# Optimization experiments

Hardware: AMD Instinct MI355X
Metric: run time of the kernel (lower is better)

## Reference

```python
import jax, jax.numpy as jnp
import numpy as np

N = 100000   # nodes
E = 1600000  # edges (avg degree 16)
DIM = 3      # coordinate dims
R = 3        # pseudo-coordinate dim
C = 32       # channels / Gaussian kernels
F = 64       # non-coordinate node features


def setup_inputs() -> dict:
    key = jax.random.key(0)
    k1, k2, k3, k4, k5 = jax.random.split(key, 5)
    features = jax.random.normal(k1, (N, DIM + F), dtype=jnp.float32)
    edge_index = jax.random.randint(k2, (E, 2), 0, N, dtype=jnp.int32)  # (row=i, col=j) per edge
    w_dense = jax.random.normal(k3, (DIM, R), dtype=jnp.float32) / jnp.sqrt(jnp.float32(DIM))  # lecun-ish
    b_dense = jnp.zeros((R,), dtype=jnp.float32)
    mu = jax.random.normal(k4, (C, N, R), dtype=jnp.float32) * 0.1
    # sigma initialized positive (abs of lecun normal in the original); keep bounded away from 0
    sig = jax.random.uniform(k5, (C, N, R), dtype=jnp.float32, minval=0.1, maxval=1.0)
    return {"features": features, "edge_index": edge_index,
            "w_dense": w_dense, "b_dense": b_dense, "mu": mu, "sig": sig}


def reference(features, edge_index, w_dense, b_dense, mu, sig):
    coords = features[:, :DIM]          # [N, 3]
    h = features[:, DIM:]               # [N, F]
    src = edge_index[:, 0]              # row index i per edge
    dst = edge_index[:, 1]              # col index j per edge
    # per-edge pseudo-coordinates: tanh(Dense_r(x_j - x_i))
    u = jnp.tanh((coords[dst] - coords[src]) @ w_dense + b_dense)      # [E, R]
    # Gaussian-mixture edge weight per (channel, edge), mu/sigma gathered at row node i
    diff = u[None, :, :] - mu[:, src, :]                               # [C, E, R]
    w = jnp.exp(-0.5 * jnp.sum(diff * diff / sig[:, src, :], axis=-1)) # [C, E]
    # (A o W) @ H summed over feature axis == sum_j w[c,i,j] * sum_f H[j,f]
    msg = w * jnp.sum(h, axis=-1)[dst][None, :]                        # [C, E]
    agg = jax.ops.segment_sum(msg.T, src, num_segments=N)              # [N, C]
    return jnp.concatenate([coords, agg], axis=-1)                     # [N, DIM + C]
```

## Files before the change

### kernel.cpp

```cpp
#include <hip/hip_runtime.h>

#define DIMV 3
#define RV 3
#define CV 32
#define ROWF 67
#define ROWO 35
#define CAP 48
#define PADSTR 49
#define SCAN_T 1024
#define NGRP 8
#define BSH 5
#define BNODES 32
#define SEGCAP 192
#define CCH 8
#define MSPAD 97

__device__ __forceinline__ float fast_tanh(float x) {
    float ex = __expf(2.0f * x);
    return (ex - 1.0f) * __builtin_amdgcn_rcpf(ex + 1.0f);
}

__device__ __forceinline__ int xcc_id() {
    int x;
    asm("s_getreg_b32 %0, hwreg(HW_REG_XCC_ID)" : "=s"(x));
    return x & (NGRP - 1);
}

__global__ void prep_kernel(const float* __restrict__ features,
                            float4* __restrict__ nd,
                            int* __restrict__ counts,
                            int* __restrict__ bcur, int nbc,
                            float* __restrict__ out, int N) {
    int gid = blockIdx.x * blockDim.x + threadIdx.x;
    if (gid < N) counts[gid] = 0;
    if (gid < nbc) bcur[gid] = 0;
    int node = gid >> 6;
    int lane = threadIdx.x & 63;
    if (node >= N) return;
    const float* row = features + (size_t)node * ROWF;
    float f0 = row[lane];
    float f1 = (lane < ROWF - 64) ? row[64 + lane] : 0.0f;
    float v = (lane >= DIMV ? f0 : 0.0f) + f1;
    for (int off = 32; off > 0; off >>= 1) v += __shfl_xor(v, off, 64);
    float c0 = __shfl(f0, 0, 64);
    float c1 = __shfl(f0, 1, 64);
    float c2 = __shfl(f0, 2, 64);
    if (lane == 0) nd[node] = make_float4(c0, c1, c2, v);
    if (lane < DIMV) out[(size_t)node * ROWO + lane] = f0;
}

__global__ void bin_kernel(const int2* __restrict__ ei2,
                           int* __restrict__ bcur,
                           unsigned int* __restrict__ bins, int E, int NB) {
    int grp = xcc_id();
    int stride = gridDim.x * blockDim.x;
    for (int e = blockIdx.x * blockDim.x + threadIdx.x; e < E; e += stride) {
        unsigned long long v =
            __builtin_nontemporal_load((const unsigned long long*)ei2 + e);
        int s = (int)(v & 0xffffffffull);
        int d = (int)(v >> 32);
        int b = s >> BSH;
        int g = grp;
        int slot = atomicAdd(bcur + g * NB + b, 1);
#pragma unroll 1
        for (int tries = 0; slot >= SEGCAP && tries < NGRP; ++tries) {
            g = (g + 1) & (NGRP - 1);
            slot = atomicAdd(bcur + g * NB + b, 1);
        }
        if (slot < SEGCAP)
            bins[(size_t)(g * NB + b) * SEGCAP + slot] =
                ((unsigned)(s & (BNODES - 1)) << 17) | (unsigned)d;
    }
}

__global__ __launch_bounds__(256, 5)
void fused_bucket_kernel(const int* __restrict__ bcur,
                         const unsigned int* __restrict__ bins,
                         const float4* __restrict__ nd,
                         const float* __restrict__ wd,
                         const float* __restrict__ bd,
                         const float* __restrict__ mu,
                         const float* __restrict__ sig,
                         float* __restrict__ out, int N, int NB) {
    __shared__ float4 ue[BNODES * PADSTR];
    __shared__ float4 snd[BNODES];
    __shared__ int lcnt[BNODES];
    __shared__ int soff[NGRP + 1];
    __shared__ float msm[CCH * MSPAD];
    __shared__ float mss[CCH * MSPAD];
    int b = blockIdx.x;
    int base = b << BSH;
    int nn = N - base; if (nn > BNODES) nn = BNODES;
    int t = threadIdx.x;
    if (t < BNODES) {
        lcnt[t] = 0;
        snd[t] = (t < nn) ? nd[base + t] : make_float4(0.f, 0.f, 0.f, 0.f);
    }
    if (t < NGRP) {
        int c = bcur[t * NB + b];
        soff[t + 1] = (c > SEGCAP) ? SEGCAP : c;
    }
    if (t == 0) soff[0] = 0;
    __syncthreads();
    if (t == 0) {
#pragma unroll
        for (int g = 0; g < NGRP; ++g) soff[g + 1] += soff[g];
    }
    __syncthreads();
    float w0 = wd[0], w1 = wd[1], w2 = wd[2];
    float w3 = wd[3], w4 = wd[4], w5 = wd[5];
    float w6 = wd[6], w7 = wd[7], w8 = wd[8];
    float b0 = bd[0], b1 = bd[1], b2 = bd[2];
    int total = soff[NGRP];
    for (int r = t; r < total; r += 256) {
        int g = 0;
#pragma unroll
        for (int gg = 1; gg < NGRP; ++gg) if (r >= soff[gg]) g = gg;
        int i = r - soff[g];
        unsigned p = bins[(size_t)(g * NB + b) * SEGCAP + i];
        int sl = p >> 17;
        int d  = p & 0x1FFFF;
        float4 pd = nd[d];
        int k = atomicAdd(&lcnt[sl], 1);
        if (k >= CAP) k = CAP - 1;
        float4 ps = snd[sl];
        float dx = pd.x - ps.x, dy = pd.y - ps.y, dz = pd.z - ps.z;
        float u0 = fast_tanh(dx * w0 + dy * w3 + dz * w6 + b0);
        float u1 = fast_tanh(dx * w1 + dy * w4 + dz * w7 + b1);
        float u2 = fast_tanh(dx * w2 + dy * w5 + dz * w8 + b2);
        ue[sl * PADSTR + k] = make_float4(u0, u1, u2, pd.w);
    }
    __syncthreads();
    int c8 = t & (CCH - 1);
    int n  = t >> 3;
    size_t slab = (size_t)N * RV;
    int cnt = 0;
    if (n < nn) { cnt = lcnt[n]; if (cnt > CAP) cnt = CAP; }
    for (int cc = 0; cc < CV / CCH; ++cc) {
        for (int f = t; f < CCH * RV * BNODES; f += 256) {
            int ci = f / (RV * BNODES);
            int j  = f - ci * (RV * BNODES);
            float vm = 0.0f, vs = 1.0f;
            if (j < nn * RV) {
                size_t gidx = (size_t)(cc * CCH + ci) * slab + (size_t)base * RV + j;
                vm = mu[gidx];
                vs = sig[gidx];
            }
            msm[ci * MSPAD + j] = vm;
            mss[ci * MSPAD + j] = vs;
        }
        __syncthreads();
        if (n < nn) {
            const float* mrow = &msm[c8 * MSPAD + n * RV];
            const float* srow = &mss[c8 * MSPAD + n * RV];
            float m0 = mrow[0], m1 = mrow[1], m2 = mrow[2];
            float i0 = __builtin_amdgcn_rcpf(srow[0]);
            float i1 = __builtin_amdgcn_rcpf(srow[1]);
            float i2 = __builtin_amdgcn_rcpf(srow[2]);
            float acc = 0.0f;
            for (int k = 0; k < cnt; ++k) {
                float4 q = ue[n * PADSTR + k];
                float d0 = q.x - m0, d1 = q.y - m1, d2 = q.z - m2;
                float t2 = d0 * d0 * i0 + d1 * d1 * i1 + d2 * d2 * i2;
                acc += __expf(-0.5f * t2) * q.w;
            }
            out[(size_t)(base + n) * ROWO + DIMV + cc * CCH + c8] = acc;
        }
        __syncthreads();
    }
}


__global__ void hist_kernel(const int2* __restrict__ ei2, int* __restrict__ counts, int E) {
    int e = blockIdx.x * blockDim.x + threadIdx.x;
    if (e >= E) return;
    atomicAdd(counts + ei2[e].x, 1);
}

__global__ void scan_a_kernel(const int* __restrict__ counts, int* __restrict__ offsets,
                              int* __restrict__ partials, int N) {
    __shared__ int sm[SCAN_T];
    int t = threadIdx.x;
    int i = blockIdx.x * SCAN_T + t;
    int c = (i < N) ? counts[i] : 0;
    sm[t] = c;
    __syncthreads();
    for (int off = 1; off < SCAN_T; off <<= 1) {
        int v = (t >= off) ? sm[t - off] : 0;
        __syncthreads();
        sm[t] += v;
        __syncthreads();
    }
    if (i < N) offsets[i] = sm[t] - c;
    if (t == SCAN_T - 1) partials[blockIdx.x] = sm[t];
}

__global__ void scan_b_kernel(int* __restrict__ partials, int B) {
    __shared__ int sm[SCAN_T];
    int t = threadIdx.x;
    int c = (t < B) ? partials[t] : 0;
    sm[t] = c;
    __syncthreads();
    for (int off = 1; off < SCAN_T; off <<= 1) {
        int v = (t >= off) ? sm[t - off] : 0;
        __syncthreads();
        sm[t] += v;
        __syncthreads();
    }
    if (t < B) partials[t] = sm[t] - c;
}

__global__ void scan_c_kernel(int* __restrict__ offsets, const int* __restrict__ partials,
                              int* __restrict__ cursor, int N, int E) {
    int i = blockIdx.x * blockDim.x + threadIdx.x;
    if (i == 0) offsets[N] = E;
    if (i >= N) return;
    int off = offsets[i] + partials[i / SCAN_T];
    offsets[i] = off;
    cursor[i] = off;
}

__global__ void scatter_u_kernel(const int2* __restrict__ ei2, int* __restrict__ cursor,
                                 const float4* __restrict__ nd,
                                 const float* __restrict__ wd, const float* __restrict__ bd,
                                 float4* __restrict__ ue, int E) {
    int e = blockIdx.x * blockDim.x + threadIdx.x;
    if (e >= E) return;
    int2 sd = ei2[e];
    int pos = atomicAdd(cursor + sd.x, 1);
    float4 ps = nd[sd.x];
    float4 pd = nd[sd.y];
    float dx = pd.x - ps.x, dy = pd.y - ps.y, dz = pd.z - ps.z;
    float u0 = fast_tanh(dx * wd[0] + dy * wd[3] + dz * wd[6] + bd[0]);
    float u1 = fast_tanh(dx * wd[1] + dy * wd[4] + dz * wd[7] + bd[1]);
    float u2 = fast_tanh(dx * wd[2] + dy * wd[5] + dz * wd[8] + bd[2]);
    ue[pos] = make_float4(u0, u1, u2, pd.w);
}

__global__ void node_acc2_kernel(const int* __restrict__ offsets,
                                 const float4* __restrict__ ue,
                                 const float* __restrict__ mu,
                                 const float* __restrict__ sig,
                                 float* __restrict__ out, int N) {
    int node = (blockIdx.x * blockDim.x + threadIdx.x) >> 6;
    if (node >= N) return;
    int lane = threadIdx.x & 63;
    int c = lane & 31;
    int half = lane >> 5;
    size_t slab = (size_t)N * RV;
    const float* mp = mu + (size_t)c * slab + (size_t)node * RV;
    const float* sp = sig + (size_t)c * slab + (size_t)node * RV;
    float m0 = mp[0], m1 = mp[1], m2 = mp[2];
    float i0 = __builtin_amdgcn_rcpf(sp[0]);
    float i1 = __builtin_amdgcn_rcpf(sp[1]);
    float i2 = __builtin_amdgcn_rcpf(sp[2]);
    int off0 = offsets[node], off1 = offsets[node + 1];
    float acc = 0.0f;
    for (int i = off0 + half; i < off1; i += 2) {
        float4 q = ue[i];
        float d0 = q.x - m0, d1 = q.y - m1, d2 = q.z - m2;
        float t = d0 * d0 * i0 + d1 * d1 * i1 + d2 * d2 * i2;
        acc += __expf(-0.5f * t) * q.w;
    }
    acc += __shfl_xor(acc, 32, 64);
    if (half == 0) out[(size_t)node * ROWO + DIMV + c] = acc;
}


__global__ void fb_pre_kernel(const float* __restrict__ features,
                              float4* __restrict__ nd, float* __restrict__ out, int N) {
    int gid = blockIdx.x * blockDim.x + threadIdx.x;
    int node = gid >> 6;
    int lane = threadIdx.x & 63;
    if (node >= N) return;
    const float* row = features + (size_t)node * ROWF;
    float f0 = row[lane];
    float f1 = (lane < ROWF - 64) ? row[64 + lane] : 0.0f;
    float v = (lane >= DIMV ? f0 : 0.0f) + f1;
    for (int off = 32; off > 0; off >>= 1) v += __shfl_xor(v, off, 64);
    float c0 = __shfl(f0, 0, 64);
    float c1 = __shfl(f0, 1, 64);
    float c2 = __shfl(f0, 2, 64);
    if (lane == 0) nd[node] = make_float4(c0, c1, c2, v);
    float* orow = out + (size_t)node * ROWO;
    if (lane < DIMV) orow[lane] = f0;
    else if (lane < ROWO) orow[lane] = 0.0f;
}

__global__ void fb_edge_kernel(const int* __restrict__ ei, const float4* __restrict__ nd,
                               const float* __restrict__ wd, const float* __restrict__ bd,
                               const float* __restrict__ mu, const float* __restrict__ sig,
                               float* __restrict__ out, int N, int E) {
    int e = blockIdx.x * blockDim.x + threadIdx.x;
    if (e >= E) return;
    int s = ei[2 * e];
    int d = ei[2 * e + 1];
    float4 ps = nd[s];
    float4 pd = nd[d];
    float dx = pd.x - ps.x, dy = pd.y - ps.y, dz = pd.z - ps.z;
    float u0 = fast_tanh(dx * wd[0] + dy * wd[3] + dz * wd[6] + bd[0]);
    float u1 = fast_tanh(dx * wd[1] + dy * wd[4] + dz * wd[7] + bd[1]);
    float u2 = fast_tanh(dx * wd[2] + dy * wd[5] + dz * wd[8] + bd[2]);
    float hs = pd.w;
    float* oagg = out + (size_t)s * ROWO + DIMV;
    size_t nodeoff = (size_t)s * RV;
    size_t slab = (size_t)N * RV;
#pragma unroll 4
    for (int c = 0; c < CV; ++c) {
        const float* mp = mu + (size_t)c * slab + nodeoff;
        const float* sp = sig + (size_t)c * slab + nodeoff;
        float d0 = u0 - mp[0], d1 = u1 - mp[1], d2 = u2 - mp[2];
        float t = d0 * d0 * __builtin_amdgcn_rcpf(sp[0])
                + d1 * d1 * __builtin_amdgcn_rcpf(sp[1])
                + d2 * d2 * __builtin_amdgcn_rcpf(sp[2]);
        atomicAdd(oagg + c, __expf(-0.5f * t) * hs);
    }
}

extern "C" void kernel_launch(void* const* d_in, const int* in_sizes, int n_in,
                              void* d_out, int out_size, void* d_ws, size_t ws_size,
                              hipStream_t stream) {
    const float* features = (const float*)d_in[0];
    const int*   ei       = (const int*)d_in[1];
    const int2*  ei2      = (const int2*)d_in[1];
    const float* wd       = (const float*)d_in[2];
    const float* bd       = (const float*)d_in[3];
    const float* mu       = (const float*)d_in[4];
    const float* sig      = (const float*)d_in[5];
    float* out = (float*)d_out;

    int N = in_sizes[0] / ROWF;
    int E = in_sizes[1] / 2;
    int B = (N + SCAN_T - 1) / SCAN_T;
    int NB = (N + BNODES - 1) / BNODES;

    size_t cur = 0;
    auto take = [&](size_t bytes) { size_t p = cur; cur += (bytes + 255) & ~(size_t)255; return p; };
    size_t o_nd      = take((size_t)N * sizeof(float4));
    size_t o_counts  = take((size_t)N * sizeof(int));
    size_t o_offsets = take((size_t)(N + 1) * sizeof(int));
    size_t o_cursor  = take((size_t)N * sizeof(int));
    size_t o_part    = take((size_t)SCAN_T * sizeof(int));
    size_t o_bcur    = take((size_t)NGRP * NB * sizeof(int));
    size_t o_bins    = take((size_t)NGRP * NB * SEGCAP * sizeof(unsigned int));
    size_t o_tail    = cur;
    size_t need_fused = o_tail;
    size_t need_full  = o_tail + (((size_t)E * sizeof(float4) + 255) & ~(size_t)255);

    char* ws = (char*)d_ws;
    float4* nd   = (float4*)(ws + o_nd);
    int* counts  = (int*)(ws + o_counts);
    int* offsets = (int*)(ws + o_offsets);
    int* cursor  = (int*)(ws + o_cursor);
    int* part    = (int*)(ws + o_part);
    int* bcur    = (int*)(ws + o_bcur);
    unsigned int* bins = (unsigned int*)(ws + o_bins);

    if (ws_size >= need_fused && N < (1 << 17)) {
        prep_kernel<<<(N + 3) / 4, 256, 0, stream>>>(features, nd, counts, bcur, NGRP * NB, out, N);
        bin_kernel<<<2048, 256, 0, stream>>>(ei2, bcur, bins, E, NB);
        fused_bucket_kernel<<<NB, 256, 0, stream>>>(bcur, bins, nd, wd, bd, mu, sig, out, N, NB);
    } else if (ws_size >= need_full && B <= SCAN_T) {
        float4* ue = (float4*)(ws + o_tail);
        prep_kernel<<<(N + 3) / 4, 256, 0, stream>>>(features, nd, counts, bcur, 0, out, N);
        hist_kernel<<<(E + 255) / 256, 256, 0, stream>>>(ei2, counts, E);
        scan_a_kernel<<<B, SCAN_T, 0, stream>>>(counts, offsets, part, N);
        scan_b_kernel<<<1, SCAN_T, 0, stream>>>(part, B);
        scan_c_kernel<<<(N + 255) / 256, 256, 0, stream>>>(offsets, part, cursor, N, E);
        scatter_u_kernel<<<(E + 255) / 256, 256, 0, stream>>>(ei2, cursor, nd, wd, bd, ue, E);
        node_acc2_kernel<<<(N + 3) / 4, 256, 0, stream>>>(offsets, ue, mu, sig, out, N);
    } else {
        fb_pre_kernel<<<(N + 3) / 4, 256, 0, stream>>>(features, nd, out, N);
        fb_edge_kernel<<<(E + 255) / 256, 256, 0, stream>>>(ei, nd, wd, bd, mu, sig, out, N, E);
    }
}
```

Measured before the change: 278.1 us.

## Compute four channels per thread with direct mu/sig loads, dropping LDS staging loop

The Gaussian-mixture phase no longer stages mu/sig through shared memory in four channel chunks with barriers. Each thread now loads its node's mu/sig for four channels straight from global memory and reuses every edge record read from shared memory across those four channels. Edge slots are XOR-swizzled by node group to cut LDS bank conflicts, and the occupancy hint rises from 5 to 6 waves. The cost is more registers per thread, and global mu/sig loads that are strided and less coalesced than the old cooperative staging.

```diff
diff --git a/kernel.cpp b/kernel.cpp
--- a/kernel.cpp
+++ b/kernel.cpp
@@ -12,8 +12,6 @@
 #define BSH 5
 #define BNODES 32
 #define SEGCAP 192
-#define CCH 8
-#define MSPAD 97
 
 __device__ __forceinline__ float fast_tanh(float x) {
     float ex = __expf(2.0f * x);
@@ -73,7 +71,7 @@
     }
 }
 
-__global__ __launch_bounds__(256, 5)
+__global__ __launch_bounds__(256, 6)
 void fused_bucket_kernel(const int* __restrict__ bcur,
                          const unsigned int* __restrict__ bins,
                          const float4* __restrict__ nd,
@@ -86,8 +84,6 @@
     __shared__ float4 snd[BNODES];
     __shared__ int lcnt[BNODES];
     __shared__ int soff[NGRP + 1];
-    __shared__ float msm[CCH * MSPAD];
-    __shared__ float mss[CCH * MSPAD];
     int b = blockIdx.x;
     int base = b << BSH;
     int nn = N - base; if (nn > BNODES) nn = BNODES;
@@ -107,66 +103,71 @@
         for (int g = 0; g < NGRP; ++g) soff[g + 1] += soff[g];
     }
     __syncthreads();
-    float w0 = wd[0], w1 = wd[1], w2 = wd[2];
-    float w3 = wd[3], w4 = wd[4], w5 = wd[5];
-    float w6 = wd[6], w7 = wd[7], w8 = wd[8];
-    float b0 = bd[0], b1 = bd[1], b2 = bd[2];
-    int total = soff[NGRP];
-    for (int r = t; r < total; r += 256) {
-        int g = 0;
-#pragma unroll
-        for (int gg = 1; gg < NGRP; ++gg) if (r >= soff[gg]) g = gg;
-        int i = r - soff[g];
-        unsigned p = bins[(size_t)(g * NB + b) * SEGCAP + i];
-        int sl = p >> 17;
-        int d  = p & 0x1FFFF;
-        float4 pd = nd[d];
-        int k = atomicAdd(&lcnt[sl], 1);
-        if (k >= CAP) k = CAP - 1;
-        float4 ps = snd[sl];
-        float dx = pd.x - ps.x, dy = pd.y - ps.y, dz = pd.z - ps.z;
-        float u0 = fast_tanh(dx * w0 + dy * w3 + dz * w6 + b0);
-        float u1 = fast_tanh(dx * w1 + dy * w4 + dz * w7 + b1);
-        float u2 = fast_tanh(dx * w2 + dy * w5 + dz * w8 + b2);
-        ue[sl * PADSTR + k] = make_float4(u0, u1, u2, pd.w);
-    }
-    __syncthreads();
-    int c8 = t & (CCH - 1);
-    int n  = t >> 3;
+    {
+        float w0 = wd[0], w1 = wd[1], w2 = wd[2];
+        float w3 = wd[3], w4 = wd[4], w5 = wd[5];
+        float w6 = wd[6], w7 = wd[7], w8 = wd[8];
+        float b0 = bd[0], b1 = bd[1], b2 = bd[2];
+        int total = soff[NGRP];
+        for (int r = t; r < total; r += 256) {
+            int g = 0;
+#pragma unroll
+            for (int gg = 1; gg < NGRP; ++gg) if (r >= soff[gg]) g = gg;
+            int i = r - soff[g];
+            unsigned p = bins[(size_t)(g * NB + b) * SEGCAP + i];
+            int sl = p >> 17;
+            int d  = p & 0x1FFFF;
+            float4 pd = nd[d];
+            int k = atomicAdd(&lcnt[sl], 1);
+            if (k >= CAP) k = CAP - 1;
+            float4 ps = snd[sl];
+            float dx = pd.x - ps.x, dy = pd.y - ps.y, dz = pd.z - ps.z;
+            float u0 = fast_tanh(dx * w0 + dy * w3 + dz * w6 + b0);
+            float u1 = fast_tanh(dx * w1 + dy * w4 + dz * w7 + b1);
+            float u2 = fast_tanh(dx * w2 + dy * w5 + dz * w8 + b2);
+            ue[sl * PADSTR + (k ^ ((sl >> 3) & 3))] = make_float4(u0, u1, u2, pd.w);
+        }
+    }
+    __syncthreads();
+    int wv = t >> 6;
+    int l  = t & 63;
+    int h  = l >> 5;
+    int n  = l & 31;
     size_t slab = (size_t)N * RV;
-    int cnt = 0;
-    if (n < nn) { cnt = lcnt[n]; if (cnt > CAP) cnt = CAP; }
-    for (int cc = 0; cc < CV / CCH; ++cc) {
-        for (int f = t; f < CCH * RV * BNODES; f += 256) {
-            int ci = f / (RV * BNODES);
-            int j  = f - ci * (RV * BNODES);
-            float vm = 0.0f, vs = 1.0f;
-            if (j < nn * RV) {
-                size_t gidx = (size_t)(cc * CCH + ci) * slab + (size_t)base * RV + j;
-                vm = mu[gidx];
-                vs = sig[gidx];
-            }
-            msm[ci * MSPAD + j] = vm;
-            mss[ci * MSPAD + j] = vs;
+    int nid = base + ((n < nn) ? n : 0);
+    float3 mv[4], sv[4];
+#pragma unroll
+    for (int j = 0; j < 4; ++j) {
+        int c = 8 * wv + 2 * j + h;
+        const float* mp = mu  + (size_t)c * slab + (size_t)nid * RV;
+        const float* sp = sig + (size_t)c * slab + (size_t)nid * RV;
+        mv[j] = *(const float3*)mp;
+        sv[j] = *(const float3*)sp;
+    }
+    float mm[4][3], im[4][3], acc[4];
+#pragma unroll
+    for (int j = 0; j < 4; ++j) {
+        mm[j][0] = mv[j].x; mm[j][1] = mv[j].y; mm[j][2] = mv[j].z;
+        im[j][0] = __builtin_amdgcn_rcpf(sv[j].x);
+        im[j][1] = __builtin_amdgcn_rcpf(sv[j].y);
+        im[j][2] = __builtin_amdgcn_rcpf(sv[j].z);
+        acc[j] = 0.0f;
+    }
+    int cnt = (n < nn) ? min(lcnt[n], CAP) : 0;
+    int key = (n >> 3) & 3;
+    for (int k = 0; k < cnt; ++k) {
+        float4 q = ue[n * PADSTR + (k ^ key)];
+#pragma unroll
+        for (int j = 0; j < 4; ++j) {
+            float d0 = q.x - mm[j][0], d1 = q.y - mm[j][1], d2 = q.z - mm[j][2];
+            float t2 = d0 * d0 * im[j][0] + d1 * d1 * im[j][1] + d2 * d2 * im[j][2];
+            acc[j] += __expf(-0.5f * t2) * q.w;
         }
-        __syncthreads();
-        if (n < nn) {
-            const float* mrow = &msm[c8 * MSPAD + n * RV];
-            const float* srow = &mss[c8 * MSPAD + n * RV];
-            float m0 = mrow[0], m1 = mrow[1], m2 = mrow[2];
-            float i0 = __builtin_amdgcn_rcpf(srow[0]);
-            float i1 = __builtin_amdgcn_rcpf(srow[1]);
-            float i2 = __builtin_amdgcn_rcpf(srow[2]);
-            float acc = 0.0f;
-            for (int k = 0; k < cnt; ++k) {
-                float4 q = ue[n * PADSTR + k];
-                float d0 = q.x - m0, d1 = q.y - m1, d2 = q.z - m2;
-                float t2 = d0 * d0 * i0 + d1 * d1 * i1 + d2 * d2 * i2;
-                acc += __expf(-0.5f * t2) * q.w;
-            }
-            out[(size_t)(base + n) * ROWO + DIMV + cc * CCH + c8] = acc;
-        }
-        __syncthreads();
+    }
+    if (n < nn) {
+        float* orow = out + (size_t)(base + n) * ROWO + DIMV;
+#pragma unroll
+        for (int j = 0; j < 4; ++j) orow[8 * wv + 2 * j + h] = acc[j];
     }
 }
 
```

Result: faster. 256.8 us (-7.7%).
